# Optimization experiments

Measured on AMD Instinct MI355X. Metric: run time of the kernel, lower is better.

Reference implementation:

```python
import jax, jax.numpy as jnp
import numpy as np

B, C, H, W = 16, 256, 48, 160
BASELINE = 0.54
REL_ELEV = 1.65
H_MEAN = 1.535


def setup_inputs() -> dict:
    key = jax.random.key(0)
    k = jax.random.split(key, 5)
    features = jax.random.normal(k[0], (B, C, H, W), dtype=jnp.float32)
    # realistic KITTI-style P2 (full-resolution intrinsics; forward divides rows 0:2 by 16)
    base = np.zeros((3, 4), np.float32)
    base[0, 0] = 721.5; base[1, 1] = 721.5
    base[0, 2] = 609.5; base[1, 2] = 172.8
    base[2, 2] = 1.0;   base[1, 3] = 0.2
    P2 = jnp.asarray(base)[None] + 0.5 * jax.random.uniform(k[1], (B, 3, 4), dtype=jnp.float32)
    w_disp = 0.05 * jax.random.normal(k[2], (1, C, 3, 3), dtype=jnp.float32)  # disp_create conv3x3
    b_disp = jnp.zeros((1,), jnp.float32)
    w_ext = 0.05 * jax.random.normal(k[3], (C, C + 1), dtype=jnp.float32)     # extract conv1x1 (O,I)
    b_ext = jnp.zeros((C,), jnp.float32)
    alpha = 0.5 * jnp.ones((1,), jnp.float32)  # nn.Parameter (init 0.0; nonzero to exercise path)
    return {"features": features, "P2": P2, "w_disp": w_disp, "b_disp": b_disp,
            "w_ext": w_ext, "b_ext": b_ext, "alpha": alpha}


def _grid_sample_border(feat, gx, gy):
    """Bilinear grid_sample, padding_mode='border', align_corners=True.
    feat: (B,C1,H,W); gx, gy: (B,H,W) in [-1,1]."""
    Bs, C1, Hs, Ws = feat.shape
    ix = jnp.clip((gx + 1.0) * 0.5 * (Ws - 1), 0.0, Ws - 1)
    iy = jnp.clip((gy + 1.0) * 0.5 * (Hs - 1), 0.0, Hs - 1)
    ix0 = jnp.floor(ix); iy0 = jnp.floor(iy)
    ix1 = jnp.minimum(ix0 + 1.0, Ws - 1); iy1 = jnp.minimum(iy0 + 1.0, Hs - 1)
    wx = (ix - ix0).reshape(Bs, 1, -1)
    wy = (iy - iy0).reshape(Bs, 1, -1)
    flat = feat.reshape(Bs, C1, Hs * Ws)

    def gather(f, yq, xq):
        idx = (yq * Ws + xq).astype(jnp.int32).reshape(-1)
        return f[:, idx]  # (C1, H*W)

    g = jax.vmap(gather)
    v00 = g(flat, iy0, ix0); v01 = g(flat, iy0, ix1)
    v10 = g(flat, iy1, ix0); v11 = g(flat, iy1, ix1)
    out = (v00 * (1 - wx) * (1 - wy) + v01 * wx * (1 - wy)
           + v10 * (1 - wx) * wy + v11 * wx * wy)
    return out.reshape(Bs, C1, Hs, Ws)


def reference(features, P2, w_disp, b_disp, w_ext, b_ext, alpha):
    x = features
    Bs = x.shape[0]
    P2 = P2.at[:, 0:2].set(P2[:, 0:2] / 16.0)
    # disp_create: conv3x3 -> tanh, then detach-scaled
    d = jax.lax.conv_general_dilated(x, w_disp, (1, 1), 'SAME',
                                     dimension_numbers=('NCHW', 'OIHW', 'NCHW'))
    d = jnp.tanh(d + b_disp[None, :, None, None])
    disp = 0.1 * (0.05 * d + 0.95 * jax.lax.stop_gradient(d))  # (B,1,H,W)

    yy = jnp.arange(H, dtype=jnp.float32)[None, :, None]  # (1,H,1): row index
    fy = P2[:, 1:2, 1:2]; cy = P2[:, 1:2, 2:3]; Ty = P2[:, 1:2, 3:4]  # (B,1,1)
    disparity = jax.nn.relu(fy * BASELINE * (yy - cy)
                            / (jnp.abs(fy * REL_ELEV + Ty) + 1e-10))  # (B,H,1)
    disparity = jnp.broadcast_to(disparity, (Bs, H, W))

    x_base = jnp.broadcast_to(jnp.linspace(-1.0, 1.0, W, dtype=jnp.float32)[None, None, :], (Bs, H, W))
    y_base = jnp.linspace(-1.0, 1.0, H, dtype=jnp.float32)[None, :, None]  # (1,H,1)
    y_shifts_base = jax.nn.relu(H_MEAN * (yy - cy) / (2.0 * (REL_ELEV - 0.5 * H_MEAN))) / (H * 0.5)
    y_shifts = y_shifts_base + disp[:, 0]  # (B,H,W)
    gy = y_base + y_shifts

    feats = jnp.concatenate([disparity[:, None], x], axis=1)  # (B,C+1,H,W)
    samp = _grid_sample_border(feats, x_base, gy)
    out = jnp.einsum('oc,bchw->bohw', w_ext, samp) + b_ext[None, :, None, None]
    return jax.nn.relu(x + out * alpha[0])
```

## Files before the change

### kernel.cpp

```cpp
#include <hip/hip_runtime.h>
#include <stdint.h>

#define NB 16
#define NC 256
#define NH 48
#define NW 160
#define HW (NH*NW)
#define NP (NB*HW)

static __device__ __forceinline__ unsigned short f2bf(float f){
  union { float f; uint32_t u; } v; v.f = f;
  uint32_t u = v.u;
  uint32_t r = (u + 0x7FFFu + ((u >> 16) & 1u)) >> 16;
  return (unsigned short)r;
}
static __device__ __forceinline__ float bf2f(unsigned short h){
  union { float f; uint32_t u; } v; v.u = ((uint32_t)h) << 16; return v.f;
}

__global__ __launch_bounds__(256) void kw_conv(const float* __restrict__ w_ext,
                                               const float* __restrict__ w_disp,
                                               unsigned short* __restrict__ WbF,
                                               unsigned short* __restrict__ WtapF){
  int d = blockIdx.x * 256 + threadIdx.x;
  if (blockIdx.x < 256){
    int j  = d & 7;
    int lane = (d >> 3) & 63;
    int mi = (d >> 9) & 3;
    int w  = (d >> 11) & 3;
    int ks = d >> 13;
    int m = w * 64 + mi * 16 + (lane & 15);
    int k = ks * 32 + (lane >> 4) * 8 + j;
    WbF[d] = f2bf(w_ext[m * 257 + 1 + k]);
  } else {
    int d2 = d - 65536;
    int j  = d2 & 7;
    int lane = (d2 >> 3) & 63;
    int ks = d2 >> 9;
    int tap = lane & 15;
    int k = ks * 32 + (lane >> 4) * 8 + j;
    WtapF[d2] = (tap < 9) ? f2bf(w_disp[k * 9 + tap]) : (unsigned short)0;
  }
}

typedef __attribute__((ext_vector_type(8))) short bf16x8;
typedef __attribute__((ext_vector_type(4))) short bf16x4;
typedef __attribute__((ext_vector_type(4))) float f32x4;

__global__ __launch_bounds__(256, 2) void kb_gemm(
    const float* __restrict__ x,
    const unsigned short* __restrict__ Wb,
    const unsigned short* __restrict__ Wtap,
    unsigned short* __restrict__ U,
    float* __restrict__ T)
{
  __shared__ __align__(16) unsigned short smem[8 * 2048];
  int bx = blockIdx.x;
  int b  = bx / 120;
  int nt = bx - b * 120;
  int p0 = nt * 64;

  int tid  = threadIdx.x;
  int lane = tid & 63;
  int w    = tid >> 6;
  int l15 = lane & 15;
  int lq  = lane >> 4;

  int q  = tid & 31;
  int cg = tid >> 5;
  const float* xs = x + ((size_t)b * NC + (size_t)cg * 32) * HW + p0 + 2 * q;

  float2 v[32];
  #pragma unroll
  for (int i = 0; i < 32; ++i)
    v[i] = *(const float2*)(xs + (size_t)i * HW);

  bf16x8 afA[4], afB[4];
  bf16x8 atA = {0,0,0,0,0,0,0,0}, atB = {0,0,0,0,0,0,0,0};
  #pragma unroll
  for (int mi = 0; mi < 4; ++mi)
    afA[mi] = *(const bf16x8*)(Wb + ((w * 4 + mi) << 9) + lane * 8);
  if (w == 0)
    atA = *(const bf16x8*)(Wtap + lane * 8);

  f32x4 zero = {0.f, 0.f, 0.f, 0.f};
  f32x4 acc[4][4];
  f32x4 acct[4];
  #pragma unroll
  for (int mi = 0; mi < 4; ++mi){
    acct[mi] = zero;
    #pragma unroll
    for (int ni = 0; ni < 4; ++ni) acc[mi][ni] = zero;
  }

  {
    int n0 = 2 * q;
    unsigned short* sw0 = smem + cg * 2048 + (n0 >> 4) * 512;
    int n15a = n0 & 15;
    #pragma unroll
    for (int g = 0; g < 4; ++g){
      unsigned short ha[8], hb[8];
      #pragma unroll
      for (int j = 0; j < 8; ++j){
        ha[j] = f2bf(v[8 * g + j].x);
        hb[j] = f2bf(v[8 * g + j].y);
      }
      *(bf16x8*)(sw0 + (n15a     + g * 16) * 8) = *(bf16x8*)ha;
      *(bf16x8*)(sw0 + (n15a + 1 + g * 16) * 8) = *(bf16x8*)hb;
    }
  }
  __syncthreads();

#define KB_STEP(T_, AFC, AFN, ATC, ATN)                                       \
  {                                                                           \
    constexpr int t_ = (T_);                                                  \
    if (t_ + 1 < 8) {                                                         \
      _Pragma("unroll")                                                       \
      for (int mi = 0; mi < 4; ++mi)                                          \
        AFN[mi] = *(const bf16x8*)(Wb + (((t_ + 1) * 16 + w * 4 + mi) << 9)   \
                                   + lane * 8);                               \
      if (w == 0)                                                             \
        ATN = *(const bf16x8*)(Wtap + ((t_ + 1) << 9) + lane * 8);            \
    }                                                                         \
    bf16x8 bg[4];                                                             \
    _Pragma("unroll")                                                         \
    for (int ni = 0; ni < 4; ++ni)                                            \
      bg[ni] = *(const bf16x8*)(smem + t_ * 2048 + ni * 512 + lane * 8);      \
    _Pragma("unroll")                                                         \
    for (int mi = 0; mi < 4; ++mi)                                            \
      _Pragma("unroll")                                                       \
      for (int ni = 0; ni < 4; ++ni)                                          \
        acc[mi][ni] = __builtin_amdgcn_mfma_f32_16x16x32_bf16(AFC[mi], bg[ni],\
                                                      acc[mi][ni], 0, 0, 0);  \
    if (w == 0) {                                                             \
      _Pragma("unroll")                                                       \
      for (int ni = 0; ni < 4; ++ni)                                          \
        acct[ni] = __builtin_amdgcn_mfma_f32_16x16x32_bf16(ATC, bg[ni],       \
                                                       acct[ni], 0, 0, 0);    \
    }                                                                         \
  }

  KB_STEP(0, afA, afB, atA, atB)
  KB_STEP(1, afB, afA, atB, atA)
  KB_STEP(2, afA, afB, atA, atB)
  KB_STEP(3, afB, afA, atB, atA)
  KB_STEP(4, afA, afB, atA, atB)
  KB_STEP(5, afB, afA, atB, atA)
  KB_STEP(6, afA, afB, atA, atB)
  KB_STEP(7, afB, afA, atB, atA)
#undef KB_STEP

  #pragma unroll
  for (int mi = 0; mi < 4; ++mi){
    int o = w * 64 + mi * 16 + lq * 4;
    #pragma unroll
    for (int ni = 0; ni < 4; ++ni){
      int n = ni * 16 + l15;
      unsigned short h[4];
      #pragma unroll
      for (int r = 0; r < 4; ++r) h[r] = f2bf(acc[mi][ni][r]);
      *(bf16x4*)(U + ((size_t)b * HW + p0 + n) * 256 + o) = *(bf16x4*)h;
    }
  }
  if (w == 0){
    #pragma unroll
    for (int ni = 0; ni < 4; ++ni){
      int n = ni * 16 + l15;
      #pragma unroll
      for (int r = 0; r < 4; ++r){
        int k = lq * 4 + r;
        if (k < 9)
          T[(size_t)k * NP + (size_t)b * HW + p0 + n] = acct[ni][r];
      }
    }
  }
}

__global__ __launch_bounds__(256) void kp_grid(
    const float* __restrict__ P2, const float* __restrict__ b_disp,
    const float* __restrict__ T, float4* __restrict__ pre)
{
  int p = blockIdx.x * 256 + threadIdx.x;
  int b  = p / HW;
  int hw = p - b * HW;
  int y  = hw / NW;
  int xx = hw - y * NW;

  float d = 0.f;
  #pragma unroll
  for (int ky = 0; ky < 3; ++ky){
    int yy2 = y + ky - 1;
    if (yy2 < 0 || yy2 >= NH) continue;
    #pragma unroll
    for (int kx = 0; kx < 3; ++kx){
      int xx2 = xx + kx - 1;
      if (xx2 < 0 || xx2 >= NW) continue;
      d += T[(size_t)(ky * 3 + kx) * NP + b * HW + yy2 * NW + xx2];
    }
  }
  float th = tanhf(d + b_disp[0]);

  float fy = P2[b * 12 + 5] * 0.0625f;
  float cy = P2[b * 12 + 6] * 0.0625f;
  float Ty = P2[b * 12 + 7] * 0.0625f;

  float ysb   = fmaxf(1.535f * ((float)y - cy) / 1.765f, 0.f) * (1.f / 24.f);
  float ybase = -1.f + (float)y * (2.f / 47.f);
  float gy = ybase + ysb + 0.1f * th;
  float iy = fminf(fmaxf((gy + 1.f) * 0.5f * 47.f, 0.f), 47.f);
  float fiy0 = floorf(iy);
  float wy = iy - fiy0;
  int iy0 = (int)fiy0;
  int iy1 = min(iy0 + 1, 47);

  float inv_den = 1.f / (fabsf(fy * 1.65f + Ty) + 1e-10f);
  float dr0 = fmaxf(fy * 0.54f * ((float)iy0 - cy) * inv_den, 0.f);
  float dr1 = fmaxf(fy * 0.54f * ((float)iy1 - cy) * inv_den, 0.f);
  float dlerp = (1.f - wy) * dr0 + wy * dr1;

  float4 pr;
  pr.x = wy; pr.y = dlerp;
  pr.z = __int_as_float(iy0 * NW + xx);
  pr.w = __int_as_float(iy1 * NW + xx);
  pre[p] = pr;
}

__global__ __launch_bounds__(256) void kc_epilogue(
    const float* __restrict__ x, const float* __restrict__ w_ext,
    const float* __restrict__ b_ext, const float* __restrict__ alpha,
    const unsigned short* __restrict__ U, const float4* __restrict__ pre,
    float* __restrict__ out)
{
  int bx = blockIdx.x;
  int ptile = bx >> 3;
  int cg    = bx & 7;
  int p = ptile * 256 + threadIdx.x;
  int b  = p / HW;
  int hw = p - b * HW;

  float4 pr = pre[p];
  float wy    = pr.x;
  float dlerp = pr.y;
  int off0 = __float_as_int(pr.z);
  int off1 = __float_as_int(pr.w);
  float w1 = 1.f - wy;
  float al = alpha[0];

  int o0 = cg * 32;
  const unsigned short* U0 = U + ((size_t)b * HW + off0) * 256 + o0;
  const unsigned short* U1 = U + ((size_t)b * HW + off1) * 256 + o0;
  bf16x8 ua[4], ub[4];
  #pragma unroll
  for (int i = 0; i < 4; ++i){
    ua[i] = *(const bf16x8*)(U0 + i * 8);
    ub[i] = *(const bf16x8*)(U1 + i * 8);
  }

  size_t base0 = (size_t)(b * NC) * HW;
  const float* xb = x + base0 + hw;
  float* ob = out + base0 + hw;

  #pragma unroll
  for (int i = 0; i < 4; ++i){
    #pragma unroll
    for (int j = 0; j < 8; ++j){
      int o = o0 + i * 8 + j;
      float u0 = bf2f((unsigned short)ua[i][j]);
      float u1 = bf2f((unsigned short)ub[i][j]);
      float val = w1 * u0 + wy * u1 + w_ext[o * 257] * dlerp + b_ext[o];
      float r = xb[(size_t)o * HW] + al * val;
      ob[(size_t)o * HW] = fmaxf(r, 0.f);
    }
  }
}

extern "C" void kernel_launch(void* const* d_in, const int* in_sizes, int n_in,
                              void* d_out, int out_size, void* d_ws, size_t ws_size,
                              hipStream_t stream) {
  const float* features = (const float*)d_in[0];
  const float* P2       = (const float*)d_in[1];
  const float* w_disp   = (const float*)d_in[2];
  const float* b_disp   = (const float*)d_in[3];
  const float* w_ext    = (const float*)d_in[4];
  const float* b_ext    = (const float*)d_in[5];
  const float* alpha    = (const float*)d_in[6];
  float* out = (float*)d_out;

  char* ws = (char*)d_ws;
  const size_t U_bytes   = (size_t)NP * 256 * 2;
  const size_t T_bytes   = (size_t)9 * NP * 4;
  const size_t pre_bytes = (size_t)NP * 16;
  unsigned short* U    = (unsigned short*)ws;
  float*          T    = (float*)(ws + U_bytes);
  float4*         pre  = (float4*)(ws + U_bytes + T_bytes);
  unsigned short* Wb   = (unsigned short*)(ws + U_bytes + T_bytes + pre_bytes);
  unsigned short* Wtap = Wb + 256 * 256;

  hipLaunchKernelGGL(kw_conv,     dim3(272),  dim3(256), 0, stream, w_ext, w_disp, Wb, Wtap);
  hipLaunchKernelGGL(kb_gemm,     dim3(1920), dim3(256), 0, stream, features, Wb, Wtap, U, T);
  hipLaunchKernelGGL(kp_grid,     dim3(480),  dim3(256), 0, stream, P2, b_disp, T, pre);
  hipLaunchKernelGGL(kc_epilogue, dim3(3840), dim3(256), 0, stream,
                     features, w_ext, b_ext, alpha, U, pre, out);
}
```

Before: 327.2 us.

## Halve GEMM pixel tile and store intermediate U in channel-group-major layout

The GEMM kernel now processes 32 pixels per block instead of 64, doubling the grid, halving shared memory and raising the occupancy hint from 2 to 4 blocks per CU. The double-buffered weight prefetch is replaced by a simple per-step load. The intermediate U tensor moves from pixel-major (256 channels contiguous per pixel) to [batch][channel-group of 4][pixel][4] layout. The epilogue's gathers then read 8-byte chunks in which neighbouring threads touch neighbouring pixels, which should coalesce better. The trade-off is that each weight fragment is re-read for twice as many blocks, and the software pipelining of weight loads is lost.

```diff
diff --git a/kernel.cpp b/kernel.cpp
--- a/kernel.cpp
+++ b/kernel.cpp
@@ -47,18 +47,18 @@
 typedef __attribute__((ext_vector_type(4))) short bf16x4;
 typedef __attribute__((ext_vector_type(4))) float f32x4;
 
-__global__ __launch_bounds__(256, 2) void kb_gemm(
+__global__ __launch_bounds__(256, 4) void kb_gemm(
     const float* __restrict__ x,
     const unsigned short* __restrict__ Wb,
     const unsigned short* __restrict__ Wtap,
     unsigned short* __restrict__ U,
     float* __restrict__ T)
 {
-  __shared__ __align__(16) unsigned short smem[8 * 2048];
+  __shared__ __align__(16) unsigned short smem[8 * 1024];
   int bx = blockIdx.x;
-  int b  = bx / 120;
-  int nt = bx - b * 120;
-  int p0 = nt * 64;
+  int b  = bx / 240;
+  int nt = bx - b * 240;
+  int p0 = nt * 32;
 
   int tid  = threadIdx.x;
   int lane = tid & 63;
@@ -66,105 +66,85 @@
   int l15 = lane & 15;
   int lq  = lane >> 4;
 
-  int q  = tid & 31;
-  int cg = tid >> 5;
-  const float* xs = x + ((size_t)b * NC + (size_t)cg * 32) * HW + p0 + 2 * q;
-
-  float2 v[32];
-  #pragma unroll
-  for (int i = 0; i < 32; ++i)
+  int q  = tid & 15;
+  int cg = tid >> 4;
+  const float* xs = x + ((size_t)b * NC + (size_t)cg * 16) * HW + p0 + 2 * q;
+
+  float2 v[16];
+  #pragma unroll
+  for (int i = 0; i < 16; ++i)
     v[i] = *(const float2*)(xs + (size_t)i * HW);
 
-  bf16x8 afA[4], afB[4];
-  bf16x8 atA = {0,0,0,0,0,0,0,0}, atB = {0,0,0,0,0,0,0,0};
-  #pragma unroll
-  for (int mi = 0; mi < 4; ++mi)
-    afA[mi] = *(const bf16x8*)(Wb + ((w * 4 + mi) << 9) + lane * 8);
-  if (w == 0)
-    atA = *(const bf16x8*)(Wtap + lane * 8);
-
   f32x4 zero = {0.f, 0.f, 0.f, 0.f};
-  f32x4 acc[4][4];
-  f32x4 acct[4];
+  f32x4 acc[4][2];
+  f32x4 acct[2];
   #pragma unroll
   for (int mi = 0; mi < 4; ++mi){
-    acct[mi] = zero;
-    #pragma unroll
-    for (int ni = 0; ni < 4; ++ni) acc[mi][ni] = zero;
-  }
+    #pragma unroll
+    for (int ni = 0; ni < 2; ++ni) acc[mi][ni] = zero;
+  }
+  acct[0] = zero; acct[1] = zero;
 
   {
-    int n0 = 2 * q;
-    unsigned short* sw0 = smem + cg * 2048 + (n0 >> 4) * 512;
-    int n15a = n0 & 15;
-    #pragma unroll
-    for (int g = 0; g < 4; ++g){
+    int ks = cg >> 1;
+    int un = q >> 3;
+    int n15a = (2 * q) & 15;
+    unsigned short* swb = smem + ks * 1024 + un * 512;
+    #pragma unroll
+    for (int g = 0; g < 2; ++g){
+      int kq = (cg * 2 + g) & 3;
       unsigned short ha[8], hb[8];
       #pragma unroll
       for (int j = 0; j < 8; ++j){
         ha[j] = f2bf(v[8 * g + j].x);
         hb[j] = f2bf(v[8 * g + j].y);
       }
-      *(bf16x8*)(sw0 + (n15a     + g * 16) * 8) = *(bf16x8*)ha;
-      *(bf16x8*)(sw0 + (n15a + 1 + g * 16) * 8) = *(bf16x8*)hb;
+      *(bf16x8*)(swb + (n15a     + kq * 16) * 8) = *(bf16x8*)ha;
+      *(bf16x8*)(swb + (n15a + 1 + kq * 16) * 8) = *(bf16x8*)hb;
     }
   }
   __syncthreads();
 
-#define KB_STEP(T_, AFC, AFN, ATC, ATN)                                       \
-  {                                                                           \
-    constexpr int t_ = (T_);                                                  \
-    if (t_ + 1 < 8) {                                                         \
-      _Pragma("unroll")                                                       \
-      for (int mi = 0; mi < 4; ++mi)                                          \
-        AFN[mi] = *(const bf16x8*)(Wb + (((t_ + 1) * 16 + w * 4 + mi) << 9)   \
-                                   + lane * 8);                               \
-      if (w == 0)                                                             \
-        ATN = *(const bf16x8*)(Wtap + ((t_ + 1) << 9) + lane * 8);            \
-    }                                                                         \
-    bf16x8 bg[4];                                                             \
-    _Pragma("unroll")                                                         \
-    for (int ni = 0; ni < 4; ++ni)                                            \
-      bg[ni] = *(const bf16x8*)(smem + t_ * 2048 + ni * 512 + lane * 8);      \
-    _Pragma("unroll")                                                         \
-    for (int mi = 0; mi < 4; ++mi)                                            \
-      _Pragma("unroll")                                                       \
-      for (int ni = 0; ni < 4; ++ni)                                          \
-        acc[mi][ni] = __builtin_amdgcn_mfma_f32_16x16x32_bf16(AFC[mi], bg[ni],\
-                                                      acc[mi][ni], 0, 0, 0);  \
-    if (w == 0) {                                                             \
-      _Pragma("unroll")                                                       \
-      for (int ni = 0; ni < 4; ++ni)                                          \
-        acct[ni] = __builtin_amdgcn_mfma_f32_16x16x32_bf16(ATC, bg[ni],       \
-                                                       acct[ni], 0, 0, 0);    \
-    }                                                                         \
-  }
-
-  KB_STEP(0, afA, afB, atA, atB)
-  KB_STEP(1, afB, afA, atB, atA)
-  KB_STEP(2, afA, afB, atA, atB)
-  KB_STEP(3, afB, afA, atB, atA)
-  KB_STEP(4, afA, afB, atA, atB)
-  KB_STEP(5, afB, afA, atB, atA)
-  KB_STEP(6, afA, afB, atA, atB)
-  KB_STEP(7, afB, afA, atB, atA)
-#undef KB_STEP
+  #pragma unroll
+  for (int t = 0; t < 8; ++t){
+    bf16x8 af[4];
+    #pragma unroll
+    for (int mi = 0; mi < 4; ++mi)
+      af[mi] = *(const bf16x8*)(Wb + ((t * 16 + w * 4 + mi) << 9) + lane * 8);
+    bf16x8 bg[2];
+    #pragma unroll
+    for (int ni = 0; ni < 2; ++ni)
+      bg[ni] = *(const bf16x8*)(smem + t * 1024 + ni * 512 + lane * 8);
+    #pragma unroll
+    for (int mi = 0; mi < 4; ++mi)
+      #pragma unroll
+      for (int ni = 0; ni < 2; ++ni)
+        acc[mi][ni] = __builtin_amdgcn_mfma_f32_16x16x32_bf16(af[mi], bg[ni],
+                                                      acc[mi][ni], 0, 0, 0);
+    if (w == 0){
+      bf16x8 at = *(const bf16x8*)(Wtap + (t << 9) + lane * 8);
+      #pragma unroll
+      for (int ni = 0; ni < 2; ++ni)
+        acct[ni] = __builtin_amdgcn_mfma_f32_16x16x32_bf16(at, bg[ni],
+                                                       acct[ni], 0, 0, 0);
+    }
+  }
 
   #pragma unroll
   for (int mi = 0; mi < 4; ++mi){
-    int o = w * 64 + mi * 16 + lq * 4;
-    #pragma unroll
-    for (int ni = 0; ni < 4; ++ni){
+    int og = w * 16 + mi * 4 + lq;
+    #pragma unroll
+    for (int ni = 0; ni < 2; ++ni){
       int n = ni * 16 + l15;
       unsigned short h[4];
       #pragma unroll
       for (int r = 0; r < 4; ++r) h[r] = f2bf(acc[mi][ni][r]);
-      *(bf16x4*)(U + ((size_t)b * HW + p0 + n) * 256 + o) = *(bf16x4*)h;
+      *(bf16x4*)(U + (((size_t)b * 64 + og) * HW + p0 + n) * 4) = *(bf16x4*)h;
     }
   }
   if (w == 0){
     #pragma unroll
-    for (int ni = 0; ni < 4; ++ni){
+    for (int ni = 0; ni < 2; ++ni){
       int n = ni * 16 + l15;
       #pragma unroll
       for (int r = 0; r < 4; ++r){
@@ -246,30 +226,30 @@
   float w1 = 1.f - wy;
   float al = alpha[0];
 
-  int o0 = cg * 32;
-  const unsigned short* U0 = U + ((size_t)b * HW + off0) * 256 + o0;
-  const unsigned short* U1 = U + ((size_t)b * HW + off1) * 256 + o0;
-  bf16x8 ua[4], ub[4];
-  #pragma unroll
-  for (int i = 0; i < 4; ++i){
-    ua[i] = *(const bf16x8*)(U0 + i * 8);
-    ub[i] = *(const bf16x8*)(U1 + i * 8);
+  int og0 = cg * 8;
+  const unsigned short* Ua = U + (((size_t)b * 64 + og0) * HW) * 4;
+  bf16x4 ua[8], ub[8];
+  #pragma unroll
+  for (int i = 0; i < 8; ++i){
+    ua[i] = *(const bf16x4*)(Ua + ((size_t)i * HW + off0) * 4);
+    ub[i] = *(const bf16x4*)(Ua + ((size_t)i * HW + off1) * 4);
   }
 
   size_t base0 = (size_t)(b * NC) * HW;
   const float* xb = x + base0 + hw;
   float* ob = out + base0 + hw;
 
-  #pragma unroll
-  for (int i = 0; i < 4; ++i){
-    #pragma unroll
-    for (int j = 0; j < 8; ++j){
-      int o = o0 + i * 8 + j;
-      float u0 = bf2f((unsigned short)ua[i][j]);
-      float u1 = bf2f((unsigned short)ub[i][j]);
+  int o0 = cg * 32;
+  #pragma unroll
+  for (int i = 0; i < 8; ++i){
+    #pragma unroll
+    for (int r = 0; r < 4; ++r){
+      int o = o0 + i * 4 + r;
+      float u0 = bf2f((unsigned short)ua[i][r]);
+      float u1 = bf2f((unsigned short)ub[i][r]);
       float val = w1 * u0 + wy * u1 + w_ext[o * 257] * dlerp + b_ext[o];
-      float r = xb[(size_t)o * HW] + al * val;
-      ob[(size_t)o * HW] = fmaxf(r, 0.f);
+      float rr = xb[(size_t)o * HW] + al * val;
+      ob[(size_t)o * HW] = fmaxf(rr, 0.f);
     }
   }
 }
@@ -297,7 +277,7 @@
   unsigned short* Wtap = Wb + 256 * 256;
 
   hipLaunchKernelGGL(kw_conv,     dim3(272),  dim3(256), 0, stream, w_ext, w_disp, Wb, Wtap);
-  hipLaunchKernelGGL(kb_gemm,     dim3(1920), dim3(256), 0, stream, features, Wb, Wtap, U, T);
+  hipLaunchKernelGGL(kb_gemm,     dim3(3840), dim3(256), 0, stream, features, Wb, Wtap, U, T);
   hipLaunchKernelGGL(kp_grid,     dim3(480),  dim3(256), 0, stream, P2, b_disp, T, pre);
   hipLaunchKernelGGL(kc_epilogue, dim3(3840), dim3(256), 0, stream,
                      features, w_ext, b_ext, alpha, U, pre, out);
```

Measured after the change: 303.7 us. 7.2% less time.
